# Performance work log

Measured on AMD Instinct MI355X. Metric: run time of the kernel, lower is better.

## Reference

```python
import jax, jax.numpy as jnp
import numpy as np


def gcn_conv(x, edge_index, W, b):
    """PyG-style GCNConv: x' = D^{-1/2} (A + I) D^{-1/2} (x W) + b."""
    n = x.shape[0]
    src, dst = edge_index[0], edge_index[1]
    # add self-loops
    loops = jnp.arange(n, dtype=src.dtype)
    src = jnp.concatenate([src, loops])
    dst = jnp.concatenate([dst, loops])
    # symmetric normalization: deg counted at target (incl. self-loop)
    deg = jnp.zeros((n,), x.dtype).at[dst].add(jnp.ones((), x.dtype))
    dinv = jnp.where(deg > 0, jax.lax.rsqrt(deg), jnp.zeros((), x.dtype))
    norm = dinv[src] * dinv[dst]  # [E + N]
    h = x @ W  # [N, out] transform before aggregation (PyG order)
    out = jnp.zeros((n, W.shape[1]), x.dtype).at[dst].add(h[src] * norm[:, None])
    return out + b


def setup_inputs() -> dict:
    key = jax.random.key(0)
    ks = jax.random.split(key, 4)
    N, F_IN, HID, OUT, E = 50000, 256, 128, 64, 800000
    x = jax.random.normal(ks[0], (N, F_IN), jnp.float32)
    edge_index = jax.random.randint(ks[1], (2, E), 0, N, dtype=jnp.int64)
    W1 = jax.random.normal(ks[2], (F_IN, HID), jnp.float32) / np.sqrt(F_IN).astype(np.float32)
    b1 = jnp.zeros((HID,), jnp.float32)
    W2 = jax.random.normal(ks[3], (HID, OUT), jnp.float32) / np.sqrt(HID).astype(np.float32)
    b2 = jnp.zeros((OUT,), jnp.float32)
    return {"x": x, "edge_index": edge_index, "W1": W1, "b1": b1, "W2": W2, "b2": b2}


def reference(x, edge_index, W1, b1, W2, b2):
    # conv1 -> relu -> dropout(eval: identity) -> conv2
    h = jax.nn.relu(gcn_conv(x, edge_index, W1, b1))
    return gcn_conv(h, edge_index, W2, b2)
```

## Files before the change

### kernel.cpp

```cpp
#include <hip/hip_runtime.h>


typedef __attribute__((ext_vector_type(8))) short bf16x8;
typedef __attribute__((ext_vector_type(4))) float f32x4;

__device__ __forceinline__ unsigned short f2bf_rne(float f) {
    unsigned u = __float_as_uint(f);
    u = u + 0x7fffu + ((u >> 16) & 1u);
    return (unsigned short)(u >> 16);
}

__device__ __forceinline__ float4 bf4f(ushort4 u) {
    float4 r;
    r.x = __uint_as_float((unsigned)u.x << 16);
    r.y = __uint_as_float((unsigned)u.y << 16);
    r.z = __uint_as_float((unsigned)u.z << 16);
    r.w = __uint_as_float((unsigned)u.w << 16);
    return r;
}

__global__ void k_wprep(const float* __restrict__ W, unsigned short* __restrict__ Wt_hi,
                        unsigned short* __restrict__ Wt_lo, int K, int N) {
    int id = blockIdx.x * blockDim.x + threadIdx.x;
    if (id < K * N) {
        int k = id / N, nn = id - k * N;
        float f = W[id];
        unsigned short h = f2bf_rne(f);
        float hf = __uint_as_float((unsigned)h << 16);
        Wt_hi[(size_t)nn * K + k] = h;
        Wt_lo[(size_t)nn * K + k] = f2bf_rne(f - hf);
    }
}

__global__ void k_init(const int* __restrict__ e32, int* __restrict__ flag,
                       int* __restrict__ cnt, int n) {
    int i = blockIdx.x * blockDim.x + threadIdx.x;
    if (i < n) cnt[i] = 0;
    if (blockIdx.x == 0 && threadIdx.x < 64) {
        int v = e32[2 * threadIdx.x + 1];
        unsigned long long ball = __ballot(v == 0);
        if (threadIdx.x == 0) flag[0] = (ball == ~0ull) ? 1 : 0;
    }
}

__device__ __forceinline__ int edge_at(const int* __restrict__ e32, long long idx, int is64) {
    return is64 ? e32[2 * idx] : e32[(int)idx];
}

__global__ void k_count(const int* __restrict__ e32, const int* __restrict__ flag,
                        int* __restrict__ cnt, int E) {
    int is64 = flag[0];
    int e = blockIdx.x * blockDim.x + threadIdx.x;
    if (e < E) {
        int d = edge_at(e32, (long long)E + e, is64);
        atomicAdd(&cnt[d], 1);
    }
}

#define SCB 256
#define SCE 8
#define SCTILE (SCB * SCE)

__global__ __launch_bounds__(SCB) void k_scan1(const int* __restrict__ cnt,
                                               int* __restrict__ blksum, int n) {
    __shared__ int red[SCB];
    int t = threadIdx.x;
    int base = blockIdx.x * SCTILE + t * SCE;
    int s = 0;
    if (base + SCE <= n) {
        int4 a = *reinterpret_cast<const int4*>(&cnt[base]);
        int4 b = *reinterpret_cast<const int4*>(&cnt[base + 4]);
        s = a.x + a.y + a.z + a.w + b.x + b.y + b.z + b.w;
    } else {
        for (int i = 0; i < SCE; ++i) { int idx = base + i; if (idx < n) s += cnt[idx]; }
    }
    red[t] = s;
    __syncthreads();
    for (int off = SCB / 2; off > 0; off >>= 1) {
        if (t < off) red[t] += red[t + off];
        __syncthreads();
    }
    if (t == 0) blksum[blockIdx.x] = red[0];
}

__global__ __launch_bounds__(SCB) void k_scan2(int* __restrict__ blksum, int nb) {
    __shared__ int red[SCB];
    int t = threadIdx.x;
    int v = (t < nb) ? blksum[t] : 0;
    red[t] = v;
    __syncthreads();
    for (int off = 1; off < SCB; off <<= 1) {
        int x = (t >= off) ? red[t - off] : 0;
        __syncthreads();
        red[t] += x;
        __syncthreads();
    }
    if (t < nb) blksum[t] = red[t] - v;
}

__global__ __launch_bounds__(SCB) void k_scan3(const int* __restrict__ cnt,
                                               const int* __restrict__ blksum,
                                               int* __restrict__ rowptr,
                                               float* __restrict__ dinv,
                                               int* __restrict__ cursor,
                                               int n, int E) {
    __shared__ int red[SCB];
    int t = threadIdx.x;
    int base = blockIdx.x * SCTILE + t * SCE;
    int v[SCE];
    int s = 0;
    if (base + SCE <= n) {
        int4 a = *reinterpret_cast<const int4*>(&cnt[base]);
        int4 b = *reinterpret_cast<const int4*>(&cnt[base + 4]);
        v[0] = a.x; v[1] = a.y; v[2] = a.z; v[3] = a.w;
        v[4] = b.x; v[5] = b.y; v[6] = b.z; v[7] = b.w;
        s = v[0] + v[1] + v[2] + v[3] + v[4] + v[5] + v[6] + v[7];
    } else {
        for (int i = 0; i < SCE; ++i) {
            int idx = base + i;
            v[i] = (idx < n) ? cnt[idx] : 0;
            s += v[i];
        }
    }
    red[t] = s;
    __syncthreads();
    for (int off = 1; off < SCB; off <<= 1) {
        int x = (t >= off) ? red[t - off] : 0;
        __syncthreads();
        red[t] += x;
        __syncthreads();
    }
    int run = red[t] - s + blksum[blockIdx.x];
    #pragma unroll
    for (int i = 0; i < SCE; ++i) {
        int idx = base + i;
        if (idx < n) {
            rowptr[idx] = run;
            dinv[idx]   = rsqrtf(1.0f + (float)v[i]);
            cursor[idx] = 0;
            run += v[i];
        }
    }
    if (blockIdx.x == 0 && t == 0) rowptr[n] = E;
}

__global__ void k_fill(const int* __restrict__ e32, const int* __restrict__ flag,
                       const int* __restrict__ rowptr, int* __restrict__ cursor,
                       int* __restrict__ esrc, int E) {
    int is64 = flag[0];
    int e = blockIdx.x * blockDim.x + threadIdx.x;
    if (e < E) {
        int s = edge_at(e32, e, is64);
        int d = edge_at(e32, (long long)E + e, is64);
        int pos = rowptr[d] + atomicAdd(&cursor[d], 1);
        esrc[pos] = s;
    }
}

template<int K, int N>
__global__ __launch_bounds__(256) void k_gemm_mfma(const float* __restrict__ A,
        const unsigned short* __restrict__ Wt_hi, const unsigned short* __restrict__ Wt_lo,
        const float* __restrict__ dinv, unsigned short* __restrict__ Hb, int n) {
    constexpr int NT  = N / 16;
    constexpr int LDA = 40;
    __shared__ unsigned short Ah[64 * LDA], Al[64 * LDA];
    __shared__ unsigned short Wh[N * LDA],  Wl[N * LDA];
    int t = threadIdx.x;
    int w = t >> 6, l = t & 63;
    int row0 = blockIdx.x * 64;
    int lrow = l & 15, lk = (l >> 4) * 8;
    f32x4 acc[NT];
    #pragma unroll
    for (int i = 0; i < NT; ++i) acc[i] = (f32x4){0.f, 0.f, 0.f, 0.f};

    for (int k0 = 0; k0 < K; k0 += 32) {
        {
            int r = t >> 2, kk = (t & 3) * 8;
            int grow = row0 + r;
            float v[8] = {0.f, 0.f, 0.f, 0.f, 0.f, 0.f, 0.f, 0.f};
            if (grow < n) {
                float4 x0 = *reinterpret_cast<const float4*>(&A[(size_t)grow * K + k0 + kk]);
                float4 x1 = *reinterpret_cast<const float4*>(&A[(size_t)grow * K + k0 + kk + 4]);
                v[0] = x0.x; v[1] = x0.y; v[2] = x0.z; v[3] = x0.w;
                v[4] = x1.x; v[5] = x1.y; v[6] = x1.z; v[7] = x1.w;
            }
            unsigned short h8[8], l8[8];
            #pragma unroll
            for (int i = 0; i < 8; ++i) {
                unsigned short h = f2bf_rne(v[i]);
                h8[i] = h;
                l8[i] = f2bf_rne(v[i] - __uint_as_float((unsigned)h << 16));
            }
            *reinterpret_cast<bf16x8*>(&Ah[r * LDA + kk]) = *reinterpret_cast<const bf16x8*>(h8);
            *reinterpret_cast<bf16x8*>(&Al[r * LDA + kk]) = *reinterpret_cast<const bf16x8*>(l8);
        }
        for (int c = t; c < N * 4; c += 256) {
            int nn = c >> 2, part = (c & 3) * 8;
            *reinterpret_cast<bf16x8*>(&Wh[nn * LDA + part]) =
                *reinterpret_cast<const bf16x8*>(&Wt_hi[(size_t)nn * K + k0 + part]);
            *reinterpret_cast<bf16x8*>(&Wl[nn * LDA + part]) =
                *reinterpret_cast<const bf16x8*>(&Wt_lo[(size_t)nn * K + k0 + part]);
        }
        __syncthreads();
        bf16x8 ah = *reinterpret_cast<const bf16x8*>(&Ah[(w * 16 + lrow) * LDA + lk]);
        bf16x8 al = *reinterpret_cast<const bf16x8*>(&Al[(w * 16 + lrow) * LDA + lk]);
        #pragma unroll
        for (int tt = 0; tt < NT; ++tt) {
            bf16x8 bh = *reinterpret_cast<const bf16x8*>(&Wh[(tt * 16 + lrow) * LDA + lk]);
            bf16x8 bl = *reinterpret_cast<const bf16x8*>(&Wl[(tt * 16 + lrow) * LDA + lk]);
            acc[tt] = __builtin_amdgcn_mfma_f32_16x16x32_bf16(ah, bh, acc[tt], 0, 0, 0);
            acc[tt] = __builtin_amdgcn_mfma_f32_16x16x32_bf16(al, bh, acc[tt], 0, 0, 0);
            acc[tt] = __builtin_amdgcn_mfma_f32_16x16x32_bf16(ah, bl, acc[tt], 0, 0, 0);
        }
        __syncthreads();
    }
    #pragma unroll
    for (int i = 0; i < 4; ++i) {
        int grow = row0 + w * 16 + (l >> 4) * 4 + i;
        if (grow < n) {
            float dv = dinv[grow];
            #pragma unroll
            for (int tt = 0; tt < NT; ++tt)
                Hb[(size_t)grow * N + tt * 16 + lrow] = f2bf_rne(acc[tt][i] * dv);
        }
    }
}

template<int LPN, bool RELU>
__global__ __launch_bounds__(256) void k_aggb(const unsigned short* __restrict__ Hb,
                                              const float* __restrict__ dinv,
                                              const int* __restrict__ rowptr,
                                              const int* __restrict__ esrc,
                                              const float* __restrict__ bias,
                                              float* __restrict__ O, int n) {
    constexpr int NF = LPN * 4;
    int grp  = threadIdx.x / LPN;
    int lane = threadIdx.x % LPN;
    int node = blockIdx.x * (256 / LPN) + grp;
    if (node >= n) return;
    int f = lane * 4;
    float dn = dinv[node];
    float4 acc = bf4f(*reinterpret_cast<const ushort4*>(&Hb[(size_t)node * NF + f]));
    int lo = rowptr[node], hi = rowptr[node + 1];
    int e = lo;
    for (; e + 8 <= hi; e += 8) {
        int s0 = esrc[e+0], s1 = esrc[e+1], s2 = esrc[e+2], s3 = esrc[e+3];
        int s4 = esrc[e+4], s5 = esrc[e+5], s6 = esrc[e+6], s7 = esrc[e+7];
        float4 v0 = bf4f(*reinterpret_cast<const ushort4*>(&Hb[(size_t)s0 * NF + f]));
        float4 v1 = bf4f(*reinterpret_cast<const ushort4*>(&Hb[(size_t)s1 * NF + f]));
        float4 v2 = bf4f(*reinterpret_cast<const ushort4*>(&Hb[(size_t)s2 * NF + f]));
        float4 v3 = bf4f(*reinterpret_cast<const ushort4*>(&Hb[(size_t)s3 * NF + f]));
        float4 v4 = bf4f(*reinterpret_cast<const ushort4*>(&Hb[(size_t)s4 * NF + f]));
        float4 v5 = bf4f(*reinterpret_cast<const ushort4*>(&Hb[(size_t)s5 * NF + f]));
        float4 v6 = bf4f(*reinterpret_cast<const ushort4*>(&Hb[(size_t)s6 * NF + f]));
        float4 v7 = bf4f(*reinterpret_cast<const ushort4*>(&Hb[(size_t)s7 * NF + f]));
        acc.x += ((v0.x + v1.x) + (v2.x + v3.x)) + ((v4.x + v5.x) + (v6.x + v7.x));
        acc.y += ((v0.y + v1.y) + (v2.y + v3.y)) + ((v4.y + v5.y) + (v6.y + v7.y));
        acc.z += ((v0.z + v1.z) + (v2.z + v3.z)) + ((v4.z + v5.z) + (v6.z + v7.z));
        acc.w += ((v0.w + v1.w) + (v2.w + v3.w)) + ((v4.w + v5.w) + (v6.w + v7.w));
    }
    for (; e < hi; ++e) {
        float4 v = bf4f(*reinterpret_cast<const ushort4*>(&Hb[(size_t)esrc[e] * NF + f]));
        acc.x += v.x; acc.y += v.y; acc.z += v.z; acc.w += v.w;
    }
    float4 bv = *reinterpret_cast<const float4*>(&bias[f]);
    acc.x = acc.x * dn + bv.x;
    acc.y = acc.y * dn + bv.y;
    acc.z = acc.z * dn + bv.z;
    acc.w = acc.w * dn + bv.w;
    if (RELU) {
        acc.x = fmaxf(acc.x, 0.f); acc.y = fmaxf(acc.y, 0.f);
        acc.z = fmaxf(acc.z, 0.f); acc.w = fmaxf(acc.w, 0.f);
    }
    *reinterpret_cast<float4*>(&O[(size_t)node * NF + f]) = acc;
}

extern "C" void kernel_launch(void* const* d_in, const int* in_sizes, int n_in,
                              void* d_out, int out_size, void* d_ws, size_t ws_size,
                              hipStream_t stream) {
    const float* x   = (const float*)d_in[0];
    const int*   e32 = (const int*)d_in[1];
    const float* W1  = (const float*)d_in[2];
    const float* b1  = (const float*)d_in[3];
    const float* W2  = (const float*)d_in[4];
    const float* b2  = (const float*)d_in[5];
    float* out = (float*)d_out;

    const int HID  = in_sizes[3];
    const int FIN  = in_sizes[2] / HID;
    const int N    = in_sizes[0] / FIN;
    const int E    = in_sizes[1] / 2;
    const int OUT  = in_sizes[5];
    (void)n_in; (void)out_size; (void)ws_size;

    char* ws = (char*)d_ws;
    size_t off = 0;
    auto take = [&](size_t bytes) -> void* {
        void* p = ws + off;
        off += (bytes + 255) & ~(size_t)255;
        return p;
    };
    int*            flag   = (int*)            take(4);
    float*          dinv   = (float*)          take((size_t)N * 4);
    int*            cnt    = (int*)            take((size_t)N * 4);
    int*            rowptr = (int*)            take((size_t)(N + 1) * 4);
    int*            blksum = (int*)            take((size_t)SCB * 4);
    unsigned short* w1h    = (unsigned short*) take((size_t)FIN * HID * 2);
    unsigned short* w1l    = (unsigned short*) take((size_t)FIN * HID * 2);
    unsigned short* w2h    = (unsigned short*) take((size_t)HID * OUT * 2);
    unsigned short* w2l    = (unsigned short*) take((size_t)HID * OUT * 2);
    int*            esrc   = (int*)            take((size_t)E * 4);
    unsigned short* h1b    = (unsigned short*) take((size_t)N * HID * 2);
    float*          agg1   = (float*)          take((size_t)N * HID * 4);
    unsigned short* h2b    = (unsigned short*) take((size_t)N * OUT * 2);

    int gN  = (N + 255) / 256;
    int gE  = (E + 255) / 256;
    int gS  = (N + SCTILE - 1) / SCTILE;
    int gM  = (N + 63) / 64;
    int gW1 = (FIN * HID + 255) / 256;
    int gW2 = (HID * OUT + 255) / 256;
    int gA1 = (N + 7) / 8;
    int gA2 = (N + 15) / 16;

    k_wprep <<<gW1, 256, 0, stream>>>(W1, w1h, w1l, FIN, HID);
    k_wprep <<<gW2, 256, 0, stream>>>(W2, w2h, w2l, HID, OUT);
    k_init  <<<gN,  256, 0, stream>>>(e32, flag, cnt, N);
    k_count <<<gE,  256, 0, stream>>>(e32, flag, cnt, E);
    k_scan1 <<<gS,  SCB, 0, stream>>>(cnt, blksum, N);
    k_scan2 <<<1,   SCB, 0, stream>>>(blksum, gS);
    k_scan3 <<<gS,  SCB, 0, stream>>>(cnt, blksum, rowptr, dinv, cnt, N, E);
    k_fill  <<<gE,  256, 0, stream>>>(e32, flag, rowptr, cnt, esrc, E);
    k_gemm_mfma<256, 128><<<gM, 256, 0, stream>>>(x, w1h, w1l, dinv, h1b, N);
    k_aggb<32, true> <<<gA1, 256, 0, stream>>>(h1b, dinv, rowptr, esrc, b1, agg1, N);
    k_gemm_mfma<128, 64> <<<gM, 256, 0, stream>>>(agg1, w2h, w2l, dinv, h2b, N);
    k_aggb<16, false><<<gA2, 256, 0, stream>>>(h2b, dinv, rowptr, esrc, b2, out, N);
}
```

Measured before the change: 271.1 us.

## Record edge rank during counting and store layer-1 activations as bf16

The count kernel now stores each edge's destination and its atomic rank in a packed word. The fill kernel then places edges without a second pass of atomics and without resetting the cursor. Layer-1 aggregation writes bf16 instead of fp32, and a new GEMM reads the bf16 A directly using two MFMAs per tile instead of three. This halves the intermediate write and read traffic, at the cost of some precision in the second-layer input. The 17-bit destination field assumes N < 131072.

Result: faster. 238.6 us (-12.0%).

```diff
diff --git a/kernel.cpp b/kernel.cpp
--- a/kernel.cpp
+++ b/kernel.cpp
@@ -48,12 +48,13 @@
 }
 
 __global__ void k_count(const int* __restrict__ e32, const int* __restrict__ flag,
-                        int* __restrict__ cnt, int E) {
+                        int* __restrict__ cnt, unsigned* __restrict__ packed, int E) {
     int is64 = flag[0];
     int e = blockIdx.x * blockDim.x + threadIdx.x;
     if (e < E) {
         int d = edge_at(e32, (long long)E + e, is64);
-        atomicAdd(&cnt[d], 1);
+        int r = atomicAdd(&cnt[d], 1);
+        packed[e] = (unsigned)d | ((unsigned)r << 17);
     }
 }
 
@@ -102,7 +103,6 @@
                                                const int* __restrict__ blksum,
                                                int* __restrict__ rowptr,
                                                float* __restrict__ dinv,
-                                               int* __restrict__ cursor,
                                                int n, int E) {
     __shared__ int red[SCB];
     int t = threadIdx.x;
@@ -137,7 +137,6 @@
         if (idx < n) {
             rowptr[idx] = run;
             dinv[idx]   = rsqrtf(1.0f + (float)v[i]);
-            cursor[idx] = 0;
             run += v[i];
         }
     }
@@ -145,15 +144,16 @@
 }
 
 __global__ void k_fill(const int* __restrict__ e32, const int* __restrict__ flag,
-                       const int* __restrict__ rowptr, int* __restrict__ cursor,
+                       const int* __restrict__ rowptr, const unsigned* __restrict__ packed,
                        int* __restrict__ esrc, int E) {
     int is64 = flag[0];
     int e = blockIdx.x * blockDim.x + threadIdx.x;
     if (e < E) {
         int s = edge_at(e32, e, is64);
-        int d = edge_at(e32, (long long)E + e, is64);
-        int pos = rowptr[d] + atomicAdd(&cursor[d], 1);
-        esrc[pos] = s;
+        unsigned p = packed[e];
+        int d = (int)(p & 0x1FFFFu);
+        int r = (int)(p >> 17);
+        esrc[rowptr[d] + r] = s;
     }
 }
 
@@ -226,13 +226,67 @@
     }
 }
 
-template<int LPN, bool RELU>
+template<int K, int N>
+__global__ __launch_bounds__(256) void k_gemm_bf16A(const unsigned short* __restrict__ A,
+        const unsigned short* __restrict__ Wt_hi, const unsigned short* __restrict__ Wt_lo,
+        const float* __restrict__ dinv, unsigned short* __restrict__ Hb, int n) {
+    constexpr int NT  = N / 16;
+    constexpr int LDA = 40;
+    __shared__ unsigned short Ah[64 * LDA];
+    __shared__ unsigned short Wh[N * LDA], Wl[N * LDA];
+    int t = threadIdx.x;
+    int w = t >> 6, l = t & 63;
+    int row0 = blockIdx.x * 64;
+    int lrow = l & 15, lk = (l >> 4) * 8;
+    f32x4 acc[NT];
+    #pragma unroll
+    for (int i = 0; i < NT; ++i) acc[i] = (f32x4){0.f, 0.f, 0.f, 0.f};
+
+    for (int k0 = 0; k0 < K; k0 += 32) {
+        {
+            int r = t >> 2, kk = (t & 3) * 8;
+            int grow = row0 + r;
+            bf16x8 v = {};
+            if (grow < n) v = *reinterpret_cast<const bf16x8*>(&A[(size_t)grow * K + k0 + kk]);
+            *reinterpret_cast<bf16x8*>(&Ah[r * LDA + kk]) = v;
+        }
+        for (int c = t; c < N * 4; c += 256) {
+            int nn = c >> 2, part = (c & 3) * 8;
+            *reinterpret_cast<bf16x8*>(&Wh[nn * LDA + part]) =
+                *reinterpret_cast<const bf16x8*>(&Wt_hi[(size_t)nn * K + k0 + part]);
+            *reinterpret_cast<bf16x8*>(&Wl[nn * LDA + part]) =
+                *reinterpret_cast<const bf16x8*>(&Wt_lo[(size_t)nn * K + k0 + part]);
+        }
+        __syncthreads();
+        bf16x8 ah = *reinterpret_cast<const bf16x8*>(&Ah[(w * 16 + lrow) * LDA + lk]);
+        #pragma unroll
+        for (int tt = 0; tt < NT; ++tt) {
+            bf16x8 bh = *reinterpret_cast<const bf16x8*>(&Wh[(tt * 16 + lrow) * LDA + lk]);
+            bf16x8 bl = *reinterpret_cast<const bf16x8*>(&Wl[(tt * 16 + lrow) * LDA + lk]);
+            acc[tt] = __builtin_amdgcn_mfma_f32_16x16x32_bf16(ah, bh, acc[tt], 0, 0, 0);
+            acc[tt] = __builtin_amdgcn_mfma_f32_16x16x32_bf16(ah, bl, acc[tt], 0, 0, 0);
+        }
+        __syncthreads();
+    }
+    #pragma unroll
+    for (int i = 0; i < 4; ++i) {
+        int grow = row0 + w * 16 + (l >> 4) * 4 + i;
+        if (grow < n) {
+            float dv = dinv[grow];
+            #pragma unroll
+            for (int tt = 0; tt < NT; ++tt)
+                Hb[(size_t)grow * N + tt * 16 + lrow] = f2bf_rne(acc[tt][i] * dv);
+        }
+    }
+}
+
+template<int LPN, bool RELU, bool OUT_BF16>
 __global__ __launch_bounds__(256) void k_aggb(const unsigned short* __restrict__ Hb,
                                               const float* __restrict__ dinv,
                                               const int* __restrict__ rowptr,
                                               const int* __restrict__ esrc,
                                               const float* __restrict__ bias,
-                                              float* __restrict__ O, int n) {
+                                              void* __restrict__ Optr, int n) {
     constexpr int NF = LPN * 4;
     int grp  = threadIdx.x / LPN;
     int lane = threadIdx.x % LPN;
@@ -272,7 +326,12 @@
         acc.x = fmaxf(acc.x, 0.f); acc.y = fmaxf(acc.y, 0.f);
         acc.z = fmaxf(acc.z, 0.f); acc.w = fmaxf(acc.w, 0.f);
     }
-    *reinterpret_cast<float4*>(&O[(size_t)node * NF + f]) = acc;
+    if (OUT_BF16) {
+        ushort4 o = { f2bf_rne(acc.x), f2bf_rne(acc.y), f2bf_rne(acc.z), f2bf_rne(acc.w) };
+        *reinterpret_cast<ushort4*>(&((unsigned short*)Optr)[(size_t)node * NF + f]) = o;
+    } else {
+        *reinterpret_cast<float4*>(&((float*)Optr)[(size_t)node * NF + f]) = acc;
+    }
 }
 
 extern "C" void kernel_launch(void* const* d_in, const int* in_sizes, int n_in,
@@ -309,9 +368,10 @@
     unsigned short* w1l    = (unsigned short*) take((size_t)FIN * HID * 2);
     unsigned short* w2h    = (unsigned short*) take((size_t)HID * OUT * 2);
     unsigned short* w2l    = (unsigned short*) take((size_t)HID * OUT * 2);
+    unsigned*       packed = (unsigned*)       take((size_t)E * 4);
     int*            esrc   = (int*)            take((size_t)E * 4);
     unsigned short* h1b    = (unsigned short*) take((size_t)N * HID * 2);
-    float*          agg1   = (float*)          take((size_t)N * HID * 4);
+    unsigned short* agg1b  = (unsigned short*) take((size_t)N * HID * 2);
     unsigned short* h2b    = (unsigned short*) take((size_t)N * OUT * 2);
 
     int gN  = (N + 255) / 256;
@@ -326,13 +386,13 @@
     k_wprep <<<gW1, 256, 0, stream>>>(W1, w1h, w1l, FIN, HID);
     k_wprep <<<gW2, 256, 0, stream>>>(W2, w2h, w2l, HID, OUT);
     k_init  <<<gN,  256, 0, stream>>>(e32, flag, cnt, N);
-    k_count <<<gE,  256, 0, stream>>>(e32, flag, cnt, E);
+    k_count <<<gE,  256, 0, stream>>>(e32, flag, cnt, packed, E);
     k_scan1 <<<gS,  SCB, 0, stream>>>(cnt, blksum, N);
     k_scan2 <<<1,   SCB, 0, stream>>>(blksum, gS);
-    k_scan3 <<<gS,  SCB, 0, stream>>>(cnt, blksum, rowptr, dinv, cnt, N, E);
-    k_fill  <<<gE,  256, 0, stream>>>(e32, flag, rowptr, cnt, esrc, E);
+    k_scan3 <<<gS,  SCB, 0, stream>>>(cnt, blksum, rowptr, dinv, N, E);
+    k_fill  <<<gE,  256, 0, stream>>>(e32, flag, rowptr, packed, esrc, E);
     k_gemm_mfma<256, 128><<<gM, 256, 0, stream>>>(x, w1h, w1l, dinv, h1b, N);
-    k_aggb<32, true> <<<gA1, 256, 0, stream>>>(h1b, dinv, rowptr, esrc, b1, agg1, N);
-    k_gemm_mfma<128, 64> <<<gM, 256, 0, stream>>>(agg1, w2h, w2l, dinv, h2b, N);
-    k_aggb<16, false><<<gA2, 256, 0, stream>>>(h2b, dinv, rowptr, esrc, b2, out, N);
-}
+    k_aggb<32, true,  true> <<<gA1, 256, 0, stream>>>(h1b, dinv, rowptr, esrc, b1, agg1b, N);
+    k_gemm_bf16A<128, 64><<<gM, 256, 0, stream>>>(agg1b, w2h, w2l, dinv, h2b, N);
+    k_aggb<16, false, false><<<gA2, 256, 0, stream>>>(h2b, dinv, rowptr, esrc, b2, out, N);
+}
```
